# Kernel optimization log

Hardware: AMD Instinct MI355X
Metric: run time of the kernel (lower is better)

## Reference

```python
import jax, jax.numpy as jnp
import numpy as np

EPROJS = 512
ODIM = 600
DLAYERS = 2
DUNITS = 512
EMBED_DIM = 512
JOINT_DIM = 512
BLANK = 0


def setup_inputs() -> dict:
    key = jax.random.key(0)
    ks = jax.random.split(key, 20)
    B, T, U = 16, 200, 64
    s_d = 1.0 / np.sqrt(DUNITS)
    s_e = 1.0 / np.sqrt(EPROJS)
    s_j = 1.0 / np.sqrt(JOINT_DIM)
    inp = {
        "hs_pad": jax.random.normal(ks[0], (B, T, EPROJS), dtype=jnp.float32),
        "ys_in_pad": jax.random.randint(ks[1], (B, U), 0, ODIM),
        "embed_table": jax.random.normal(ks[2], (ODIM, EMBED_DIM), dtype=jnp.float32).at[BLANK].set(0.0),
        # LSTMCell layer 0: input EMBED_DIM -> DUNITS (gates i,f,g,o stacked => 4*DUNITS)
        "W_ih0": jax.random.uniform(ks[3], (4 * DUNITS, EMBED_DIM), minval=-s_d, maxval=s_d),
        "W_hh0": jax.random.uniform(ks[4], (4 * DUNITS, DUNITS), minval=-s_d, maxval=s_d),
        "b_ih0": jax.random.uniform(ks[5], (4 * DUNITS,), minval=-s_d, maxval=s_d),
        "b_hh0": jax.random.uniform(ks[6], (4 * DUNITS,), minval=-s_d, maxval=s_d),
        # LSTMCell layer 1: DUNITS -> DUNITS
        "W_ih1": jax.random.uniform(ks[7], (4 * DUNITS, DUNITS), minval=-s_d, maxval=s_d),
        "W_hh1": jax.random.uniform(ks[8], (4 * DUNITS, DUNITS), minval=-s_d, maxval=s_d),
        "b_ih1": jax.random.uniform(ks[9], (4 * DUNITS,), minval=-s_d, maxval=s_d),
        "b_hh1": jax.random.uniform(ks[10], (4 * DUNITS,), minval=-s_d, maxval=s_d),
        # joint network
        "W_enc": jax.random.uniform(ks[11], (JOINT_DIM, EPROJS), minval=-s_e, maxval=s_e),
        "b_enc": jax.random.uniform(ks[12], (JOINT_DIM,), minval=-s_e, maxval=s_e),
        "W_dec": jax.random.uniform(ks[13], (JOINT_DIM, DUNITS), minval=-s_d, maxval=s_d),
        "W_out": jax.random.uniform(ks[14], (ODIM, JOINT_DIM), minval=-s_j, maxval=s_j),
        "b_out": jax.random.uniform(ks[15], (ODIM,), minval=-s_j, maxval=s_j),
    }
    return inp


def _lstm_cell(x, h, c, W_ih, W_hh, b_ih, b_hh):
    gates = x @ W_ih.T + b_ih + h @ W_hh.T + b_hh  # (B, 4*D)
    i, f, g, o = jnp.split(gates, 4, axis=-1)
    c_new = jax.nn.sigmoid(f) * c + jax.nn.sigmoid(i) * jnp.tanh(g)
    h_new = jax.nn.sigmoid(o) * jnp.tanh(c_new)
    return h_new, c_new


def _decode(eys, W_ih0, W_hh0, b_ih0, b_hh0, W_ih1, W_hh1, b_ih1, b_hh1):
    # eys: (B, U, E). Sequential 2-layer LSTM over U via scan.
    B = eys.shape[0]
    z = jnp.zeros((B, DUNITS), dtype=eys.dtype)
    carry0 = (z, z, z, z)  # h0, c0, h1, c1

    def step(carry, ey):
        h0, c0, h1, c1 = carry
        h0, c0 = _lstm_cell(ey, h0, c0, W_ih0, W_hh0, b_ih0, b_hh0)
        h1, c1 = _lstm_cell(h0, h1, c1, W_ih1, W_hh1, b_ih1, b_hh1)
        return (h0, c0, h1, c1), h1

    _, h_dec = jax.lax.scan(step, carry0, jnp.swapaxes(eys, 0, 1))  # (U, B, D)
    return jnp.swapaxes(h_dec, 0, 1)  # (B, U, D)


def reference(hs_pad, ys_in_pad, embed_table, W_ih0, W_hh0, b_ih0, b_hh0,
              W_ih1, W_hh1, b_ih1, b_hh1, W_enc, b_enc, W_dec, W_out, b_out):
    eys = embed_table[ys_in_pad]  # (B, U, E); dropout = identity at p=0
    h_dec = _decode(eys, W_ih0, W_hh0, b_ih0, b_hh0, W_ih1, W_hh1, b_ih1, b_hh1)
    # Joint: project BEFORE broadcasting (thin GEMMs), then broadcast-add.
    enc_p = hs_pad @ W_enc.T + b_enc            # (B, T, J)
    dec_p = h_dec @ W_dec.T                     # (B, U, J)
    z = jnp.tanh(enc_p[:, :, None, :] + dec_p[:, None, :, :])  # (B, T, U, J)
    return z @ W_out.T + b_out                  # (B, T, U, odim)
```

## Files before the change

### kernel.cpp

```cpp
#include <hip/hip_runtime.h>
#include <hip/hip_bf16.h>
#include <stdint.h>

#define DEVI __device__ __forceinline__

typedef unsigned short u16;
typedef __attribute__((ext_vector_type(8))) short short8;
typedef __attribute__((ext_vector_type(4))) float f32x4;
typedef __attribute__((ext_vector_type(16))) float f32x16;

DEVI u16 f2bf(float f) {
  union { float f; uint32_t u; } v; v.f = f;
  return (u16)((v.u + 0x7fffu + ((v.u >> 16) & 1u)) >> 16);
}
DEVI float tanh_c(float x) {
  float e = __expf(x + x);
  float r = __builtin_amdgcn_rcpf(e + 1.0f);
  return __builtin_fmaf(-2.0f, r, 1.0f);
}
DEVI float sigm(float x) { return __builtin_amdgcn_rcpf(1.0f + __expf(-x)); }
DEVI uint32_t tj2(float a, float b) {
  float ea = __expf(a + a), eb = __expf(b + b);
  float ta = __builtin_fmaf(-2.0f, __builtin_amdgcn_rcpf(ea + 1.0f), 1.0f);
  float tb = __builtin_fmaf(-2.0f, __builtin_amdgcn_rcpf(eb + 1.0f), 1.0f);
  union { __hip_bfloat162 h; uint32_t u; } cv;
  cv.h = __float22bfloat162_rn(make_float2(ta, tb));
  return cv.u;
}

__global__ void prep_kernel(
    const float* __restrict__ W_ih0, const float* __restrict__ W_hh0,
    const float* __restrict__ W_ih1, const float* __restrict__ W_hh1,
    const float* __restrict__ W_enc, const float* __restrict__ W_dec,
    const float* __restrict__ W_out, const float* __restrict__ embed,
    const float* __restrict__ hs_pad,
    const float* __restrict__ b_ih0, const float* __restrict__ b_hh0,
    const float* __restrict__ b_ih1, const float* __restrict__ b_hh1,
    const float* __restrict__ b_out,
    u16* __restrict__ Wih0b, u16* __restrict__ Whh0b,
    u16* __restrict__ Wih1b, u16* __restrict__ Whh1b,
    u16* __restrict__ Wencb, u16* __restrict__ Wdecb,
    u16* __restrict__ embedb, u16* __restrict__ hsb,
    u16* __restrict__ Wshufb,
    float* __restrict__ bsum0, float* __restrict__ bsum1, float* __restrict__ boutp)
{
  const int c1 = 1048576, c2 = 2097152, c3 = 3145728, c4 = 4194304;
  const int c5 = 4456448, c6 = 4718592, c7 = 5025792, c8 = 6664192;
  const int c9 = 6991872, c10 = 6993920, c11 = 6995968, c12 = 6996608;
  for (int i = blockIdx.x * blockDim.x + threadIdx.x; i < c12; i += gridDim.x * blockDim.x) {
    if (i < c1)       Wih0b[i]      = f2bf(W_ih0[i]);
    else if (i < c2)  Whh0b[i - c1] = f2bf(W_hh0[i - c1]);
    else if (i < c3)  Wih1b[i - c2] = f2bf(W_ih1[i - c2]);
    else if (i < c4)  Whh1b[i - c3] = f2bf(W_hh1[i - c3]);
    else if (i < c5)  Wencb[i - c4] = f2bf(W_enc[i - c4]);
    else if (i < c6)  Wdecb[i - c5] = f2bf(W_dec[i - c5]);
    else if (i < c7)  embedb[i - c6] = f2bf(embed[i - c6]);
    else if (i < c8)  hsb[i - c7]   = f2bf(hs_pad[i - c7]);
    else if (i < c9) {
      int e = i - c8;
      int kc = e / 10240, r = e % 10240;
      int tile = r >> 9, r2 = r & 511;
      int lane = r2 >> 3, ii = r2 & 7;
      int n = tile * 32 + (lane & 31);
      int k = kc * 16 + ((lane >> 5) << 3) + ii;
      Wshufb[e] = (n < 600) ? f2bf(W_out[n * 512 + k]) : (u16)0;
    }
    else if (i < c10) { int n = i - c9;  bsum0[n] = b_ih0[n] + b_hh0[n]; }
    else if (i < c11) { int n = i - c10; bsum1[n] = b_ih1[n] + b_hh1[n]; }
    else              { int n = i - c11; boutp[n] = (n < 600) ? b_out[n] : 0.0f; }
  }
}

__global__ __launch_bounds__(256) void gemm_bf16(
    const u16* __restrict__ A, const u16* __restrict__ B,
    const int* __restrict__ ys, const float* __restrict__ bias,
    float* __restrict__ out, int N, int mode)
{
  int tid = threadIdx.x, wv = tid >> 6, l = tid & 63;
  int m0 = blockIdx.x * 64, n0 = blockIdx.y * 64;
  int row = m0 + wv * 16 + (l & 15);
  const u16* arow;
  if (mode == 1) { int uu = row >> 4, bb = row & 15; arow = A + (size_t)ys[bb * 64 + uu] * 512; }
  else           arow = A + (size_t)row * 512;
  int kof = (l >> 4) * 8;
  arow += kof;
  const u16* br = B + (size_t)(n0 + (l & 15)) * 512 + kof;
  f32x4 a0 = {0.f,0.f,0.f,0.f}, a1 = a0, a2 = a0, a3 = a0;
  for (int kk = 0; kk < 512; kk += 32) {
    short8 av = *(const short8*)(arow + kk);
    short8 b0 = *(const short8*)(br + kk);
    short8 b1 = *(const short8*)(br + 8192 + kk);
    short8 b2 = *(const short8*)(br + 16384 + kk);
    short8 b3 = *(const short8*)(br + 24576 + kk);
    a0 = __builtin_amdgcn_mfma_f32_16x16x32_bf16(av, b0, a0, 0, 0, 0);
    a1 = __builtin_amdgcn_mfma_f32_16x16x32_bf16(av, b1, a1, 0, 0, 0);
    a2 = __builtin_amdgcn_mfma_f32_16x16x32_bf16(av, b2, a2, 0, 0, 0);
    a3 = __builtin_amdgcn_mfma_f32_16x16x32_bf16(av, b3, a3, 0, 0, 0);
  }
  int col = l & 15, rb = m0 + wv * 16 + (l >> 4) * 4;
  f32x4 accs[4] = {a0, a1, a2, a3};
#pragma unroll
  for (int g = 0; g < 4; ++g) {
    int n = n0 + g * 16 + col;
    float bs = bias ? bias[n] : 0.0f;
#pragma unroll
    for (int i2 = 0; i2 < 4; ++i2)
      out[(size_t)(rb + i2) * N + n] = accs[g][i2] + bs;
  }
}

#define L0WG 32
#define NWGT 96

DEVI short8 ald16(const u16* p) {
  union { unsigned long long q[2]; short8 v; } u;
  u.q[0] = __hip_atomic_load((unsigned long long*)p,       __ATOMIC_RELAXED, __HIP_MEMORY_SCOPE_AGENT);
  u.q[1] = __hip_atomic_load((unsigned long long*)(p + 4), __ATOMIC_RELAXED, __HIP_MEMORY_SCOPE_AGENT);
  return u.v;
}
DEVI void waitflags(const int* f0, const int* f1, int n0, int n1) {
  if (threadIdx.x < 64) {
    int l = threadIdx.x;
    for (;;) {
      int a = __hip_atomic_load((int*)(f0 + (l & 31) * 16), __ATOMIC_RELAXED, __HIP_MEMORY_SCOPE_AGENT);
      int b = __hip_atomic_load((int*)(f1 + l * 16),        __ATOMIC_RELAXED, __HIP_MEMORY_SCOPE_AGENT);
      if (__all(a >= n0 && b >= n1)) break;
      __builtin_amdgcn_s_sleep(1);
    }
    __builtin_amdgcn_fence(__ATOMIC_ACQUIRE, "agent");
  }
  __syncthreads();
}
DEVI void postflag(int* slot, int val) {
  __syncthreads();
  if (threadIdx.x == 0) {
    asm volatile("s_waitcnt vmcnt(0)" ::: "memory");
    __hip_atomic_store(slot, val, __ATOMIC_RELAXED, __HIP_MEMORY_SCOPE_AGENT);
  }
}
DEVI const u16* haddr(const u16* base, int slot, int k, int b) {
  return base + slot * 8192 + (k >> 4) * 256 + b * 16 + (k & 15);
}
DEVI void hstore(u16* base, int idx, u16 mine, int tid) {
  int other = __shfl_xor((int)mine, 1);
  if (!(tid & 1)) {
    uint32_t pkv = (uint32_t)mine | (((uint32_t)other & 0xffffu) << 16);
    __hip_atomic_store((uint32_t*)(base + idx), pkv, __ATOMIC_RELAXED, __HIP_MEMORY_SCOPE_AGENT);
  }
}

__global__ __launch_bounds__(256) void lstm_kernel(
    const float* __restrict__ Xg0,
    const u16* __restrict__ Whh0, const u16* __restrict__ Wih1, const u16* __restrict__ Whh1,
    const float* __restrict__ bsum1,
    u16* __restrict__ h0b, u16* __restrict__ h1b,
    u16* __restrict__ Hdec,
    int* __restrict__ flags0, int* __restrict__ flags1)
{
  __shared__ float red[16][256];
  const int bid = blockIdx.x, tid = threadIdx.x;
  const int wv = tid >> 6, l = tid & 63;
  const int lb = l & 15, kof = (l >> 4) * 8;
  const int drb = (l >> 4) * 4;

  if (bid < L0WG) {
    const int be = tid >> 4, je = tid & 15, jg = (bid << 4) + je;
    short8 breg[16];
#pragma unroll
    for (int g = 0; g < 4; ++g) {
      const u16* bp = Whh0 + (size_t)(g * 512 + bid * 16 + lb) * 512 + wv * 128 + kof;
#pragma unroll
      for (int ks = 0; ks < 4; ++ks)
        breg[g * 4 + ks] = *(const short8*)(bp + ks * 32);
    }
    float c0 = 0.f;
    for (int t = 0; t < 64; ++t) {
      const float* xg = Xg0 + (size_t)((t << 4) + be) * 2048 + jg;
      float x0 = xg[0], x1 = xg[512], x2 = xg[1024], x3 = xg[1536];
      waitflags(flags0, flags1, t, (t > 7) ? (t - 7) : 0);
      const int rs = (t + 7) & 7;
      f32x4 g0 = {0.f,0.f,0.f,0.f}, g1 = g0, g2 = g0, g3 = g0;
#pragma unroll
      for (int ks = 0; ks < 4; ++ks) {
        int kk = wv * 128 + ks * 32 + kof;
        short8 av = ald16(haddr(h0b, rs, kk, lb));
        g0 = __builtin_amdgcn_mfma_f32_16x16x32_bf16(av, breg[0 * 4 + ks], g0, 0, 0, 0);
        g1 = __builtin_amdgcn_mfma_f32_16x16x32_bf16(av, breg[1 * 4 + ks], g1, 0, 0, 0);
        g2 = __builtin_amdgcn_mfma_f32_16x16x32_bf16(av, breg[2 * 4 + ks], g2, 0, 0, 0);
        g3 = __builtin_amdgcn_mfma_f32_16x16x32_bf16(av, breg[3 * 4 + ks], g3, 0, 0, 0);
      }
      f32x4 gs[4] = {g0, g1, g2, g3};
#pragma unroll
      for (int g = 0; g < 4; ++g)
#pragma unroll
        for (int i2 = 0; i2 < 4; ++i2)
          red[wv * 4 + g][(drb + i2) * 16 + lb] = gs[g][i2];
      __syncthreads();
      {
        float s0 = 0, s1 = 0, s2 = 0, s3 = 0;
#pragma unroll
        for (int v2 = 0; v2 < 4; ++v2) {
          s0 += red[v2 * 4 + 0][be * 16 + je]; s1 += red[v2 * 4 + 1][be * 16 + je];
          s2 += red[v2 * 4 + 2][be * 16 + je]; s3 += red[v2 * 4 + 3][be * 16 + je];
        }
        float gi = s0 + x0, gf = s1 + x1, gg = s2 + x2, go = s3 + x3;
        float I = sigm(gi), F = sigm(gf), G = tanh_c(gg), O = sigm(go);
        c0 = F * c0 + I * G;
        float h0 = O * tanh_c(c0);
        hstore(h0b, ((t & 7) * 32 + bid) * 256 + (tid & ~1), f2bf(h0), tid);
      }
      postflag(flags0 + bid * 16, t + 1);
    }
  } else {
    const int v = bid - L0WG;
    const u16* base0 = (wv < 2) ? Wih1 : Whh1;
    const int kbase = (wv & 1) * 256;
    short8 breg[16];
#pragma unroll
    for (int tt = 0; tt < 2; ++tt) {
      int c = tt * 16 + lb, gate = c >> 3, du = c & 7;
      const u16* bp = base0 + (size_t)(gate * 512 + v * 8 + du) * 512 + kbase + kof;
#pragma unroll
      for (int ks = 0; ks < 8; ++ks)
        breg[tt * 8 + ks] = *(const short8*)(bp + ks * 32);
    }
    float bs0 = 0, bs1 = 0, bs2 = 0, bs3 = 0, c1 = 0.f;
    if (tid < 128) {
      int du = tid & 7, ju = v * 8 + du;
      bs0 = bsum1[ju]; bs1 = bsum1[512 + ju]; bs2 = bsum1[1024 + ju]; bs3 = bsum1[1536 + ju];
    }
    for (int t = 0; t < 64; ++t) {
      waitflags(flags0, flags1, t + 1, t);
      const u16* hsrc = (wv < 2) ? (h0b + (t & 7) * 8192) : (h1b + ((t + 7) & 7) * 8192);
      f32x4 g0 = {0.f,0.f,0.f,0.f}, g1 = g0;
#pragma unroll
      for (int ks = 0; ks < 8; ++ks) {
        int kk = kbase + ks * 32 + kof;
        short8 av = ald16(hsrc + (kk >> 4) * 256 + lb * 16 + (kk & 15));
        g0 = __builtin_amdgcn_mfma_f32_16x16x32_bf16(av, breg[0 * 8 + ks], g0, 0, 0, 0);
        g1 = __builtin_amdgcn_mfma_f32_16x16x32_bf16(av, breg[1 * 8 + ks], g1, 0, 0, 0);
      }
#pragma unroll
      for (int i2 = 0; i2 < 4; ++i2) {
        red[wv * 2 + 0][(drb + i2) * 16 + lb] = g0[i2];
        red[wv * 2 + 1][(drb + i2) * 16 + lb] = g1[i2];
      }
      __syncthreads();
      u16 hb = 0; int be = 0, ju = 0;
      if (tid < 128) {
        be = tid >> 3; int du = tid & 7; ju = v * 8 + du;
        float sg[4] = {bs0, bs1, bs2, bs3};
#pragma unroll
        for (int g = 0; g < 4; ++g) {
          int c = g * 8 + du, tt = c >> 4, cc = c & 15;
          float acc = 0.f;
#pragma unroll
          for (int w2 = 0; w2 < 4; ++w2) acc += red[w2 * 2 + tt][be * 16 + cc];
          sg[g] += acc;
        }
        float I = sigm(sg[0]), F = sigm(sg[1]), G = tanh_c(sg[2]), O = sigm(sg[3]);
        c1 = F * c1 + I * G;
        float h1v = O * tanh_c(c1);
        hb = f2bf(h1v);
        int idx = ((t & 7) * 32 + (ju >> 4)) * 256 + be * 16 + (ju & 15);
        hstore(h1b, idx & ~1, hb, tid);
      }
      postflag(flags1 + v * 16, t + 1);
      if (tid < 128) Hdec[(size_t)((t << 4) + be) * 512 + ju] = hb;
    }
  }
}

__global__ __launch_bounds__(256) void joint_kernel(
    const float* __restrict__ enc_p,
    const float* __restrict__ dec_p,
    const u16* __restrict__ Wshuf,
    const float* __restrict__ boutp,
    float* __restrict__ out)
{
  __shared__ int4 wlds[2][1280];
  __shared__ int4 zlds[2][256];
  int bid = blockIdx.x;
  int b = bid / 400, rem = bid % 400;
  int tb = rem / 8, rem2 = rem % 8;
  int ub = rem2 >> 1, nh = rem2 & 1;
  int tid = threadIdx.x, wv = tid >> 6, l = tid & 63;
  int mv = wv >> 1, nv = wv & 1;
  int ln31 = l & 31, lh = l >> 5;
  const int tile0 = nv * 5;
  f32x16 acc[5];
#pragma unroll
  for (int j = 0; j < 5; ++j) {
    float bv = boutp[nh * 320 + (tile0 + j) * 32 + ln31];
#pragma unroll
    for (int g = 0; g < 16; ++g) acc[j][g] = bv;
  }
  int zr = tid & 63, zg = tid >> 6;
  const float* er = enc_p + (size_t)(b * 200 + tb * 4 + (zr >> 4)) * 512 + zg * 8;
  const float* dr = dec_p + (size_t)((ub * 16 + (zr & 15)) * 16 + b) * 512 + zg * 8;
  const int zslot = ((zg >> 1) * 2 + (zr >> 5)) * 64 + ((zg & 1) << 5) + (zr & 31);
  const int4* gW = (const int4*)Wshuf;
  const int nhof = nh * 640;
  const int L0 = tid, L1 = 256 + tid, L2 = 512 + tid + ((tid >= 128) ? 640 : 0),
            L3 = 1408 + tid, L4 = 1664 + tid;
  const int S2 = 512 + tid;

  int4 aw0, aw1, aw2, aw3, aw4; float4 ae0, ae1, ad0, ad1;
  int4 bw0, bw1, bw2, bw3, bw4; float4 be0, be1, bd0, bd1;

  {
    int4 w0 = gW[nhof + L0], w1 = gW[nhof + L1], w2 = gW[nhof + L2],
         w3 = gW[nhof + L3], w4 = gW[nhof + L4];
    float4 e0 = *(const float4*)(er),     e1 = *(const float4*)(er + 4);
    float4 d0 = *(const float4*)(dr),     d1 = *(const float4*)(dr + 4);
    const int cb1 = 2560 + nhof;
    aw0 = gW[cb1 + L0]; aw1 = gW[cb1 + L1]; aw2 = gW[cb1 + L2];
    aw3 = gW[cb1 + L3]; aw4 = gW[cb1 + L4];
    ae0 = *(const float4*)(er + 32); ae1 = *(const float4*)(er + 36);
    ad0 = *(const float4*)(dr + 32); ad1 = *(const float4*)(dr + 36);
    int4 pk;
    pk.x = (int)tj2(e0.x + d0.x, e0.y + d0.y);
    pk.y = (int)tj2(e0.z + d0.z, e0.w + d0.w);
    pk.z = (int)tj2(e1.x + d1.x, e1.y + d1.y);
    pk.w = (int)tj2(e1.z + d1.z, e1.w + d1.w);
    zlds[0][zslot] = pk;
    wlds[0][tid] = w0; wlds[0][256 + tid] = w1; wlds[0][S2] = w2;
    wlds[0][768 + tid] = w3; wlds[0][1024 + tid] = w4;
    __syncthreads();
  }

#define JBODY(C, CUR, NXT, W0, W1, W2, W3, W4, E0, E1, D0, D1,                  \
              PW0, PW1, PW2, PW3, PW4, PE0, PE1, PD0, PD1)                      \
  {                                                                             \
    if ((C) + 2 <= 15) {                                                        \
      const int cb = ((C) + 2) * 2560 + nhof;                                   \
      PW0 = gW[cb + L0]; PW1 = gW[cb + L1]; PW2 = gW[cb + L2];                  \
      PW3 = gW[cb + L3]; PW4 = gW[cb + L4];                                     \
      int k0 = ((C) + 2) * 32;                                                  \
      PE0 = *(const float4*)(er + k0); PE1 = *(const float4*)(er + k0 + 4);     \
      PD0 = *(const float4*)(dr + k0); PD1 = *(const float4*)(dr + k0 + 4);     \
    }                                                                           \
    _Pragma("unroll")                                                           \
    for (int ks = 0; ks < 2; ++ks) {                                            \
      short8 aA = *(const short8*)&zlds[CUR][(ks * 2 + mv) * 64 + l];           \
      _Pragma("unroll")                                                         \
      for (int j = 0; j < 5; ++j) {                                             \
        short8 bw = *(const short8*)&wlds[CUR][ks * 640 + (tile0 + j) * 64 + l];\
        acc[j] = __builtin_amdgcn_mfma_f32_32x32x16_bf16(aA, bw, acc[j], 0, 0, 0); \
      }                                                                         \
    }                                                                           \
    if ((C) + 1 <= 15) {                                                        \
      wlds[NXT][tid] = W0; wlds[NXT][256 + tid] = W1; wlds[NXT][S2] = W2;       \
      wlds[NXT][768 + tid] = W3; wlds[NXT][1024 + tid] = W4;                    \
      int4 pk;                                                                  \
      pk.x = (int)tj2(E0.x + D0.x, E0.y + D0.y);                                \
      pk.y = (int)tj2(E0.z + D0.z, E0.w + D0.w);                                \
      pk.z = (int)tj2(E1.x + D1.x, E1.y + D1.y);                                \
      pk.w = (int)tj2(E1.z + D1.z, E1.w + D1.w);                                \
      zlds[NXT][zslot] = pk;                                                    \
    }                                                                           \
    __syncthreads();                                                            \
  }

  for (int cc = 0; cc < 8; ++cc) {
    const int c0 = cc * 2;
    JBODY(c0,     0, 1, aw0, aw1, aw2, aw3, aw4, ae0, ae1, ad0, ad1,
                        bw0, bw1, bw2, bw3, bw4, be0, be1, bd0, bd1);
    JBODY(c0 + 1, 1, 0, bw0, bw1, bw2, bw3, bw4, be0, be1, bd0, bd1,
                        aw0, aw1, aw2, aw3, aw4, ae0, ae1, ad0, ad1);
  }
#undef JBODY

#pragma unroll
  for (int j = 0; j < 5; ++j) {
    int n = nh * 320 + (tile0 + j) * 32 + ln31;
    if (n < 600) {
      int rbase = mv * 32 + 4 * lh;
#pragma unroll
      for (int g = 0; g < 16; ++g) {
        int r = rbase + (g & 3) + ((g >> 2) << 3);
        int tt = tb * 4 + (r >> 4), uu = ub * 16 + (r & 15);
        __builtin_nontemporal_store(
            acc[j][g], &out[(size_t)((b * 200 + tt) * 64 + uu) * 600 + n]);
      }
    }
  }
}

extern "C" void kernel_launch(void* const* d_in, const int* in_sizes, int n_in,
                              void* d_out, int out_size, void* d_ws, size_t ws_size,
                              hipStream_t stream) {
  const float* hs_pad = (const float*)d_in[0];
  const int*   ys     = (const int*)d_in[1];
  const float* embed  = (const float*)d_in[2];
  const float* W_ih0  = (const float*)d_in[3];
  const float* W_hh0  = (const float*)d_in[4];
  const float* b_ih0  = (const float*)d_in[5];
  const float* b_hh0  = (const float*)d_in[6];
  const float* W_ih1  = (const float*)d_in[7];
  const float* W_hh1  = (const float*)d_in[8];
  const float* b_ih1  = (const float*)d_in[9];
  const float* b_hh1  = (const float*)d_in[10];
  const float* W_enc  = (const float*)d_in[11];
  const float* b_enc  = (const float*)d_in[12];
  const float* W_dec  = (const float*)d_in[13];
  const float* W_out  = (const float*)d_in[14];
  const float* b_out  = (const float*)d_in[15];
  float* out = (float*)d_out;

  uint8_t* ws = (uint8_t*)d_ws;
  size_t off = 0;
  auto alloc = [&](size_t bytes) -> void* {
    void* p = ws + off;
    off = (off + bytes + 255) & ~(size_t)255;
    return p;
  };
  int* flags0   = (int*)alloc(2048);
  int* flags1   = (int*)alloc(4096);
  u16* h0buf    = (u16*)alloc(8 * 32 * 256 * 2);
  u16* h1buf    = (u16*)alloc(8 * 32 * 256 * 2);
  u16* Hdec     = (u16*)alloc(64 * 16 * 512 * 2);
  float* Xg0    = (float*)alloc(1024 * 2048 * 4);
  float* enc_p  = (float*)alloc(3200 * 512 * 4);
  float* dec_p  = (float*)alloc(1024 * 512 * 4);
  u16* Wih0b    = (u16*)alloc(2048 * 512 * 2);
  u16* Whh0b    = (u16*)alloc(2048 * 512 * 2);
  u16* Wih1b    = (u16*)alloc(2048 * 512 * 2);
  u16* Whh1b    = (u16*)alloc(2048 * 512 * 2);
  u16* Wencb    = (u16*)alloc(512 * 512 * 2);
  u16* Wdecb    = (u16*)alloc(512 * 512 * 2);
  u16* embedb   = (u16*)alloc(600 * 512 * 2);
  u16* hsb      = (u16*)alloc(3200 * 512 * 2);
  u16* Wshufb   = (u16*)alloc(32 * 20 * 64 * 8 * 2);
  float* bsum0  = (float*)alloc(2048 * 4);
  float* bsum1  = (float*)alloc(2048 * 4);
  float* boutp  = (float*)alloc(640 * 4);

  (void)hipMemsetAsync(d_ws, 0, 2048 + 4096 + 131072 + 131072, stream);

  prep_kernel<<<2048, 256, 0, stream>>>(
      W_ih0, W_hh0, W_ih1, W_hh1, W_enc, W_dec, W_out, embed, hs_pad,
      b_ih0, b_hh0, b_ih1, b_hh1, b_out,
      Wih0b, Whh0b, Wih1b, Whh1b, Wencb, Wdecb, embedb, hsb, Wshufb,
      bsum0, bsum1, boutp);

  dim3 g1(16, 32);
  gemm_bf16<<<g1, 256, 0, stream>>>(embedb, Wih0b, ys, bsum0, Xg0, 2048, 1);
  dim3 g2(50, 8);
  gemm_bf16<<<g2, 256, 0, stream>>>(hsb, Wencb, nullptr, b_enc, enc_p, 512, 0);
  lstm_kernel<<<NWGT, 256, 0, stream>>>(Xg0, Whh0b, Wih1b, Whh1b, bsum1,
                                        h0buf, h1buf, Hdec, flags0, flags1);
  dim3 g3(16, 8);
  gemm_bf16<<<g3, 256, 0, stream>>>(Hdec, Wdecb, nullptr, nullptr, dec_p, 512, 0);
  joint_kernel<<<6400, 256, 0, stream>>>(enc_p, dec_p, Wshufb, boutp, out);
}
```

Before: 560.9 us.

## Fuse input/encoder/decoder GEMMs into persistent LSTM kernel with flag-based overlap

Merges the Xg0 input-projection GEMM, the encoder projection GEMM and the decoder projection GEMM into the LSTM launch as extra workgroups. Per-row-tile counters let LSTM layer 0 start a timestep as soon as its Xg0 rows are ready, and the dec_p tiles spin until LSTM layer 1 has produced the needed timesteps. This removes three kernel launches and overlaps the serial recurrence with independent GEMM work. In exchange it relies on all 96 LSTM workgroups being co-resident with the GEMM blocks and adds atomic loads and stores for the shared buffers. It also drops an explicit vmcnt wait before flag posting.

```diff
diff --git a/kernel.cpp b/kernel.cpp
--- a/kernel.cpp
+++ b/kernel.cpp
@@ -26,6 +26,12 @@
   union { __hip_bfloat162 h; uint32_t u; } cv;
   cv.h = __float22bfloat162_rn(make_float2(ta, tb));
   return cv.u;
+}
+DEVI short8 ald16(const u16* p) {
+  union { unsigned long long q[2]; short8 v; } u;
+  u.q[0] = __hip_atomic_load((unsigned long long*)p,       __ATOMIC_RELAXED, __HIP_MEMORY_SCOPE_AGENT);
+  u.q[1] = __hip_atomic_load((unsigned long long*)(p + 4), __ATOMIC_RELAXED, __HIP_MEMORY_SCOPE_AGENT);
+  return u.v;
 }
 
 __global__ void prep_kernel(
@@ -71,23 +77,22 @@
   }
 }
 
-__global__ __launch_bounds__(256) void gemm_bf16(
-    const u16* __restrict__ A, const u16* __restrict__ B,
-    const int* __restrict__ ys, const float* __restrict__ bias,
-    float* __restrict__ out, int N, int mode)
+template<int MODE, bool AAT, bool SAT>
+DEVI void gemm_tile(const u16* __restrict__ A, const u16* __restrict__ B,
+                    const int* __restrict__ ys, const float* __restrict__ bias,
+                    float* __restrict__ out, int N, int m0, int n0, int tid)
 {
-  int tid = threadIdx.x, wv = tid >> 6, l = tid & 63;
-  int m0 = blockIdx.x * 64, n0 = blockIdx.y * 64;
+  int wv = tid >> 6, l = tid & 63;
   int row = m0 + wv * 16 + (l & 15);
   const u16* arow;
-  if (mode == 1) { int uu = row >> 4, bb = row & 15; arow = A + (size_t)ys[bb * 64 + uu] * 512; }
+  if (MODE == 1) { int uu = row >> 4, bb = row & 15; arow = A + (size_t)ys[bb * 64 + uu] * 512; }
   else           arow = A + (size_t)row * 512;
   int kof = (l >> 4) * 8;
   arow += kof;
   const u16* br = B + (size_t)(n0 + (l & 15)) * 512 + kof;
   f32x4 a0 = {0.f,0.f,0.f,0.f}, a1 = a0, a2 = a0, a3 = a0;
   for (int kk = 0; kk < 512; kk += 32) {
-    short8 av = *(const short8*)(arow + kk);
+    short8 av = AAT ? ald16(arow + kk) : *(const short8*)(arow + kk);
     short8 b0 = *(const short8*)(br + kk);
     short8 b1 = *(const short8*)(br + 8192 + kk);
     short8 b2 = *(const short8*)(br + 16384 + kk);
@@ -104,27 +109,28 @@
     int n = n0 + g * 16 + col;
     float bs = bias ? bias[n] : 0.0f;
 #pragma unroll
-    for (int i2 = 0; i2 < 4; ++i2)
-      out[(size_t)(rb + i2) * N + n] = accs[g][i2] + bs;
+    for (int i2 = 0; i2 < 4; ++i2) {
+      float v = accs[g][i2] + bs;
+      if (SAT)
+        __hip_atomic_store(&out[(size_t)(rb + i2) * N + n], v,
+                           __ATOMIC_RELAXED, __HIP_MEMORY_SCOPE_AGENT);
+      else
+        out[(size_t)(rb + i2) * N + n] = v;
+    }
   }
 }
 
 #define L0WG 32
-#define NWGT 96
-
-DEVI short8 ald16(const u16* p) {
-  union { unsigned long long q[2]; short8 v; } u;
-  u.q[0] = __hip_atomic_load((unsigned long long*)p,       __ATOMIC_RELAXED, __HIP_MEMORY_SCOPE_AGENT);
-  u.q[1] = __hip_atomic_load((unsigned long long*)(p + 4), __ATOMIC_RELAXED, __HIP_MEMORY_SCOPE_AGENT);
-  return u.v;
-}
-DEVI void waitflags(const int* f0, const int* f1, int n0, int n1) {
+#define FUSED_WG 1136
+
+DEVI void waitflags(const int* f0, const int* f1, const int* xc, int n0, int n1, int xneed) {
   if (threadIdx.x < 64) {
     int l = threadIdx.x;
     for (;;) {
       int a = __hip_atomic_load((int*)(f0 + (l & 31) * 16), __ATOMIC_RELAXED, __HIP_MEMORY_SCOPE_AGENT);
       int b = __hip_atomic_load((int*)(f1 + l * 16),        __ATOMIC_RELAXED, __HIP_MEMORY_SCOPE_AGENT);
-      if (__all(a >= n0 && b >= n1)) break;
+      int c = xc ? __hip_atomic_load((int*)xc, __ATOMIC_RELAXED, __HIP_MEMORY_SCOPE_AGENT) : xneed;
+      if (__all(a >= n0 && b >= n1 && c >= xneed)) break;
       __builtin_amdgcn_s_sleep(1);
     }
     __builtin_amdgcn_fence(__ATOMIC_ACQUIRE, "agent");
@@ -133,10 +139,8 @@
 }
 DEVI void postflag(int* slot, int val) {
   __syncthreads();
-  if (threadIdx.x == 0) {
-    asm volatile("s_waitcnt vmcnt(0)" ::: "memory");
+  if (threadIdx.x == 0)
     __hip_atomic_store(slot, val, __ATOMIC_RELAXED, __HIP_MEMORY_SCOPE_AGENT);
-  }
 }
 DEVI const u16* haddr(const u16* base, int slot, int k, int b) {
   return base + slot * 8192 + (k >> 4) * 256 + b * 16 + (k & 15);
@@ -149,13 +153,18 @@
   }
 }
 
-__global__ __launch_bounds__(256) void lstm_kernel(
-    const float* __restrict__ Xg0,
+__global__ __launch_bounds__(256) void lstm_fused(
+    const u16* __restrict__ embedb, const u16* __restrict__ Wih0b,
+    const int* __restrict__ ys, const float* __restrict__ bsum0,
+    float* __restrict__ Xg0,
+    const u16* __restrict__ hsb, const u16* __restrict__ Wencb,
+    const float* __restrict__ b_enc, float* __restrict__ enc_p,
+    const u16* __restrict__ Wdecb, float* __restrict__ dec_p,
     const u16* __restrict__ Whh0, const u16* __restrict__ Wih1, const u16* __restrict__ Whh1,
     const float* __restrict__ bsum1,
     u16* __restrict__ h0b, u16* __restrict__ h1b,
     u16* __restrict__ Hdec,
-    int* __restrict__ flags0, int* __restrict__ flags1)
+    int* __restrict__ flags0, int* __restrict__ flags1, int* __restrict__ xcnt)
 {
   __shared__ float red[16][256];
   const int bid = blockIdx.x, tid = threadIdx.x;
@@ -163,6 +172,37 @@
   const int lb = l & 15, kof = (l >> 4) * 8;
   const int drb = (l >> 4) * 4;
 
+  if (bid >= 96) {
+    if (bid < 608) {
+      int g = bid - 96, mt = g >> 5, nt = g & 31;
+      gemm_tile<1, false, true>(embedb, Wih0b, ys, bsum0, Xg0, 2048,
+                                mt * 64, nt * 64, tid);
+      asm volatile("s_waitcnt vmcnt(0)" ::: "memory");
+      __syncthreads();
+      if (tid == 0)
+        __hip_atomic_fetch_add(xcnt + mt, 1, __ATOMIC_RELAXED, __HIP_MEMORY_SCOPE_AGENT);
+    } else if (bid < 1008) {
+      int g = bid - 608, mt = g >> 3, nt = g & 7;
+      gemm_tile<0, false, false>(hsb, Wencb, nullptr, b_enc, enc_p, 512,
+                                 mt * 64, nt * 64, tid);
+    } else {
+      int g = bid - 1008, mt = g >> 3, nt = g & 7;
+      const int need = mt * 4 + 4;
+      if (tid < 64) {
+        for (;;) {
+          int a = __hip_atomic_load((int*)(flags1 + tid * 16), __ATOMIC_RELAXED, __HIP_MEMORY_SCOPE_AGENT);
+          if (__all(a >= need)) break;
+          __builtin_amdgcn_s_sleep(8);
+        }
+        __builtin_amdgcn_fence(__ATOMIC_ACQUIRE, "agent");
+      }
+      __syncthreads();
+      gemm_tile<0, true, false>(Hdec, Wdecb, nullptr, nullptr, dec_p, 512,
+                                mt * 64, nt * 64, tid);
+    }
+    return;
+  }
+
   if (bid < L0WG) {
     const int be = tid >> 4, je = tid & 15, jg = (bid << 4) + je;
     short8 breg[16];
@@ -175,9 +215,12 @@
     }
     float c0 = 0.f;
     for (int t = 0; t < 64; ++t) {
+      waitflags(flags0, flags1, xcnt + (t >> 2), t, (t > 7) ? (t - 7) : 0, 32);
       const float* xg = Xg0 + (size_t)((t << 4) + be) * 2048 + jg;
-      float x0 = xg[0], x1 = xg[512], x2 = xg[1024], x3 = xg[1536];
-      waitflags(flags0, flags1, t, (t > 7) ? (t - 7) : 0);
+      float x0 = __hip_atomic_load((float*)(xg),        __ATOMIC_RELAXED, __HIP_MEMORY_SCOPE_AGENT);
+      float x1 = __hip_atomic_load((float*)(xg + 512),  __ATOMIC_RELAXED, __HIP_MEMORY_SCOPE_AGENT);
+      float x2 = __hip_atomic_load((float*)(xg + 1024), __ATOMIC_RELAXED, __HIP_MEMORY_SCOPE_AGENT);
+      float x3 = __hip_atomic_load((float*)(xg + 1536), __ATOMIC_RELAXED, __HIP_MEMORY_SCOPE_AGENT);
       const int rs = (t + 7) & 7;
       f32x4 g0 = {0.f,0.f,0.f,0.f}, g1 = g0, g2 = g0, g3 = g0;
 #pragma unroll
@@ -230,7 +273,7 @@
       bs0 = bsum1[ju]; bs1 = bsum1[512 + ju]; bs2 = bsum1[1024 + ju]; bs3 = bsum1[1536 + ju];
     }
     for (int t = 0; t < 64; ++t) {
-      waitflags(flags0, flags1, t + 1, t);
+      waitflags(flags0, flags1, nullptr, t + 1, t, 0);
       const u16* hsrc = (wv < 2) ? (h0b + (t & 7) * 8192) : (h1b + ((t + 7) & 7) * 8192);
       f32x4 g0 = {0.f,0.f,0.f,0.f}, g1 = g0;
 #pragma unroll
@@ -246,9 +289,8 @@
         red[wv * 2 + 1][(drb + i2) * 16 + lb] = g1[i2];
       }
       __syncthreads();
-      u16 hb = 0; int be = 0, ju = 0;
       if (tid < 128) {
-        be = tid >> 3; int du = tid & 7; ju = v * 8 + du;
+        int be = tid >> 3, du = tid & 7, ju = v * 8 + du;
         float sg[4] = {bs0, bs1, bs2, bs3};
 #pragma unroll
         for (int g = 0; g < 4; ++g) {
@@ -261,12 +303,12 @@
         float I = sigm(sg[0]), F = sigm(sg[1]), G = tanh_c(sg[2]), O = sigm(sg[3]);
         c1 = F * c1 + I * G;
         float h1v = O * tanh_c(c1);
-        hb = f2bf(h1v);
+        u16 hb = f2bf(h1v);
         int idx = ((t & 7) * 32 + (ju >> 4)) * 256 + be * 16 + (ju & 15);
         hstore(h1b, idx & ~1, hb, tid);
+        hstore(Hdec, ((t << 4) + be) * 512 + (ju & ~1), hb, tid);
       }
       postflag(flags1 + v * 16, t + 1);
-      if (tid < 128) Hdec[(size_t)((t << 4) + be) * 512 + ju] = hb;
     }
   }
 }
@@ -417,6 +459,7 @@
   };
   int* flags0   = (int*)alloc(2048);
   int* flags1   = (int*)alloc(4096);
+  int* xcnt     = (int*)alloc(256);
   u16* h0buf    = (u16*)alloc(8 * 32 * 256 * 2);
   u16* h1buf    = (u16*)alloc(8 * 32 * 256 * 2);
   u16* Hdec     = (u16*)alloc(64 * 16 * 512 * 2);
@@ -436,7 +479,7 @@
   float* bsum1  = (float*)alloc(2048 * 4);
   float* boutp  = (float*)alloc(640 * 4);
 
-  (void)hipMemsetAsync(d_ws, 0, 2048 + 4096 + 131072 + 131072, stream);
+  (void)hipMemsetAsync(d_ws, 0, 2048 + 4096 + 256 + 131072 + 131072, stream);
 
   prep_kernel<<<2048, 256, 0, stream>>>(
       W_ih0, W_hh0, W_ih1, W_hh1, W_enc, W_dec, W_out, embed, hs_pad,
@@ -444,13 +487,12 @@
       Wih0b, Whh0b, Wih1b, Whh1b, Wencb, Wdecb, embedb, hsb, Wshufb,
       bsum0, bsum1, boutp);
 
-  dim3 g1(16, 32);
-  gemm_bf16<<<g1, 256, 0, stream>>>(embedb, Wih0b, ys, bsum0, Xg0, 2048, 1);
-  dim3 g2(50, 8);
-  gemm_bf16<<<g2, 256, 0, stream>>>(hsb, Wencb, nullptr, b_enc, enc_p, 512, 0);
-  lstm_kernel<<<NWGT, 256, 0, stream>>>(Xg0, Whh0b, Wih1b, Whh1b, bsum1,
-                                        h0buf, h1buf, Hdec, flags0, flags1);
-  dim3 g3(16, 8);
-  gemm_bf16<<<g3, 256, 0, stream>>>(Hdec, Wdecb, nullptr, nullptr, dec_p, 512, 0);
+  lstm_fused<<<FUSED_WG, 256, 0, stream>>>(
+      embedb, Wih0b, ys, bsum0, Xg0,
+      hsb, Wencb, b_enc, enc_p,
+      Wdecb, dec_p,
+      Whh0b, Wih1b, Whh1b, bsum1,
+      h0buf, h1buf, Hdec, flags0, flags1, xcnt);
+
   joint_kernel<<<6400, 256, 0, stream>>>(enc_p, dec_p, Wshufb, boutp, out);
 }
```

Result: slower. 625.0 us (+11.4%).
